# Optimization experiments

Hardware: AMD Instinct MI355X
Metric: run time of the kernel (lower is better)

Reference implementation:

```python
import jax, jax.numpy as jnp
import numpy as np

HID = 256
EDGE_F = 64
N_CELL = 4096
N_EDGE = 65536
BSZ = 4
EPS = 1e-5


def setup_inputs() -> dict:
    key = jax.random.key(0)
    ks = jax.random.split(key, 12)
    def lin(k, fan_in, fan_out):
        # torch Linear default init: U(-1/sqrt(fan_in), 1/sqrt(fan_in))
        bound = 1.0 / np.sqrt(fan_in)
        kw, kb = jax.random.split(k)
        W = jax.random.uniform(kw, (fan_in, fan_out), jnp.float32, -bound, bound)
        b = jax.random.uniform(kb, (fan_out,), jnp.float32, -bound, bound)
        return W, b
    cell_x = jax.random.normal(ks[0], (BSZ, N_CELL, HID), jnp.float32)
    edge_index = jax.random.randint(ks[1], (BSZ, N_EDGE, 2), 0, N_CELL, jnp.int64)
    edge_attr = jax.random.normal(ks[2], (BSZ, N_EDGE, EDGE_F), jnp.float32)
    mW1, mb1 = lin(ks[3], HID + EDGE_F, HID)
    mW2, mb2 = lin(ks[4], HID, HID)
    uW1, ub1 = lin(ks[5], 2 * HID, HID)
    uW2, ub2 = lin(ks[6], HID, HID)
    gamma = jnp.ones((HID,), jnp.float32)
    beta = jnp.zeros((HID,), jnp.float32)
    return {"cell_x": cell_x, "edge_index": edge_index, "edge_attr": edge_attr,
            "mW1": mW1, "mb1": mb1, "mW2": mW2, "mb2": mb2,
            "uW1": uW1, "ub1": ub1, "uW2": uW2, "ub2": ub2,
            "gamma": gamma, "beta": beta}


def reference(cell_x, edge_index, edge_attr, mW1, mb1, mW2, mb2,
              uW1, ub1, uW2, ub2, gamma, beta):
    n_cell = cell_x.shape[1]
    src = jnp.clip(edge_index[..., 0], 0, n_cell - 1)  # [B, E]
    dst = jnp.clip(edge_index[..., 1], 0, n_cell - 1)  # [B, E]

    # gather source node features per edge: [B, E, H]
    src_x = jnp.take_along_axis(cell_x, src[..., None], axis=1)

    # edge message MLP
    m_in = jnp.concatenate([src_x, edge_attr], axis=-1)  # [B, E, H+F]
    msg = jax.nn.relu(m_in @ mW1 + mb1) @ mW2 + mb2      # [B, E, H]

    # mean aggregation at destination nodes (scatter-add + count)
    def agg_one(m, d):
        s = jax.ops.segment_sum(m, d, num_segments=n_cell)                    # [N, H]
        c = jax.ops.segment_sum(jnp.ones((d.shape[0],), m.dtype), d,
                                num_segments=n_cell)                          # [N]
        return s / jnp.maximum(c, 1.0)[:, None]
    agg = jax.vmap(agg_one)(msg, dst)  # [B, N, H]

    # node update MLP + residual LayerNorm
    u_in = jnp.concatenate([cell_x, agg], axis=-1)        # [B, N, 2H]
    out = jax.nn.relu(u_in @ uW1 + ub1) @ uW2 + ub2       # [B, N, H]
    h = cell_x + out
    mu = jnp.mean(h, axis=-1, keepdims=True)
    var = jnp.mean(jnp.square(h - mu), axis=-1, keepdims=True)
    return (h - mu) * jax.lax.rsqrt(var + EPS) * gamma + beta
```

## Files before the change

kernel.cpp:

```cpp
#include <hip/hip_runtime.h>

#define HID 256
#define EF  64
#define KIN 320
#define NC  4096
#define NE  65536
#define BSZ 4
#define EPSV 1e-5f

typedef unsigned short ushort_t;
typedef __attribute__((ext_vector_type(8))) short s16x8;
typedef __attribute__((ext_vector_type(16))) float f32x16;

#define EPAD 68
#define HPAD 260
#define UPAD 520
#define HSF  260

__device__ __forceinline__ ushort_t bf16_rne(float f) {
    unsigned u = __float_as_uint(f);
    return (ushort_t)((u + 0x7fffu + ((u >> 16) & 1u)) >> 16);
}
__device__ __forceinline__ float bf16_to_f(ushort_t u) {
    return __uint_as_float(((unsigned)u) << 16);
}
__device__ __forceinline__ void split_bf16(float v, ushort_t& h, ushort_t& l) {
    unsigned u = __float_as_uint(v);
    h = (ushort_t)(u >> 16);
    float hf = __uint_as_float(u & 0xffff0000u);
    l = (ushort_t)(__float_as_uint(v - hf) >> 16);
}

__device__ __forceinline__ void pack_one(const float* W, int idx,
                                         ushort_t* hi, ushort_t* lo) {
    int l = idx & 63;
    int tn = idx >> 6;
    int nt = tn & 7, t = tn >> 3;
    int k0 = t * 16 + (l >> 5) * 8;
    int col = nt * 32 + (l & 31);
    #pragma unroll
    for (int j = 0; j < 8; ++j) {
        float v = W[(size_t)(k0 + j) * 256 + col];
        ushort_t h, lw;
        split_bf16(v, h, lw);
        hi[(size_t)idx * 8 + j] = h;
        lo[(size_t)idx * 8 + j] = lw;
    }
}

#define FR1 10240
#define FR2 8192
#define PACK1B 104
#define FUSEB 256
#define ZEROB 256

__global__ __launch_bounds__(256)
void prep_kernel(const float* __restrict__ mW1, const float* __restrict__ uW1,
                 const float* __restrict__ uW2, const float* __restrict__ mW2,
                 const float* __restrict__ ub1, const float* __restrict__ mb2,
                 ushort_t* __restrict__ w1hi, ushort_t* __restrict__ w1lo,
                 ushort_t* __restrict__ u1hi, ushort_t* __restrict__ u1lo,
                 ushort_t* __restrict__ u2hi, ushort_t* __restrict__ u2lo,
                 float* __restrict__ W2u, float* __restrict__ bias2u,
                 float4* __restrict__ zp, int n4) {
    int bid = blockIdx.x;
    if (bid < PACK1B) {
        int idx = bid * 256 + threadIdx.x;
        if (idx < FR1) { pack_one(mW1, idx, w1hi, w1lo); return; }
        idx -= FR1;
        if (idx < FR2) { pack_one(uW1, idx, u1hi, u1lo); return; }
        idx -= FR2;
        pack_one(uW2, idx, u2hi, u2lo);
        return;
    }
    bid -= PACK1B;
    if (bid < FUSEB) {
        int k = bid, n = threadIdx.x;
        const float* wrow = mW2 + (size_t)k * 256;
        float acc = 0.f;
        #pragma unroll 8
        for (int m = 0; m < 256; ++m)
            acc = fmaf(wrow[m], uW1[(size_t)(256 + m) * 256 + n], acc);
        W2u[(size_t)k * 256 + n] = acc;
        return;
    }
    bid -= FUSEB;
    if (bid == 0) {
        int n = threadIdx.x;
        float acc = ub1[n];
        #pragma unroll 8
        for (int m = 0; m < 256; ++m)
            acc = fmaf(mb2[m], uW1[(size_t)(256 + m) * 256 + n], acc);
        bias2u[n] = acc;
        return;
    }
    bid -= 1;
    int i = bid * 256 + threadIdx.x;
    int stride = ZEROB * 256;
    float4 z = make_float4(0.f, 0.f, 0.f, 0.f);
    for (; i < n4; i += stride) zp[i] = z;
}

__global__ __launch_bounds__(256)
void hist_kernel(const int* __restrict__ eidx, float* __restrict__ counts) {
    int i = blockIdx.x * 256 + threadIdx.x;
    int b = i >> 16;
    int2 v = ((const int2*)eidx)[i];
    int d = min(max(v.y, 0), NC - 1);
    atomicAdd(&counts[b * NC + d], 1.0f);
}

__global__ __launch_bounds__(1024)
void scan_kernel(const float* __restrict__ counts, int* __restrict__ woff,
                 const float* __restrict__ W2u,
                 ushort_t* __restrict__ w2uhi, ushort_t* __restrict__ w2ulo) {
    if (blockIdx.x >= BSZ) {
        if (threadIdx.x < 256) {
            int idx = (blockIdx.x - BSZ) * 256 + threadIdx.x;
            pack_one(W2u, idx, w2uhi, w2ulo);
        }
        return;
    }
    __shared__ int wsum[16];
    int b = blockIdx.x, t = threadIdx.x;
    int base = b * NC + t * 4;
    int v0 = (int)counts[base],     v1 = (int)counts[base + 1];
    int v2 = (int)counts[base + 2], v3 = (int)counts[base + 3];
    int ts = v0 + v1 + v2 + v3;
    int lane = t & 63;
    int x = ts;
    #pragma unroll
    for (int off = 1; off < 64; off <<= 1) {
        int y = __shfl_up(x, off, 64);
        if (lane >= off) x += y;
    }
    if (lane == 63) wsum[t >> 6] = x;
    __syncthreads();
    if (t == 0) {
        int s = 0;
        #pragma unroll
        for (int w = 0; w < 16; ++w) { int tmp = wsum[w]; wsum[w] = s; s += tmp; }
    }
    __syncthreads();
    int excl = wsum[t >> 6] + (x - ts);
    woff[base]     = excl;
    woff[base + 1] = excl + v0;
    woff[base + 2] = excl + v0 + v1;
    woff[base + 3] = excl + v0 + v1 + v2;
}

__global__ __launch_bounds__(256)
void scatter_kernel(const int* __restrict__ eidx, int* __restrict__ woff,
                    int* __restrict__ sorted) {
    int i = blockIdx.x * 256 + threadIdx.x;
    int b = i >> 16, e = i & (NE - 1);
    int2 v = ((const int2*)eidx)[i];
    int d = min(max(v.y, 0), NC - 1);
    int pos = atomicAdd(&woff[b * NC + d], 1);
    sorted[(size_t)b * NE + pos] = e;
}

__global__ __launch_bounds__(512, 6)
void pre_kernel(const float* __restrict__ cell_x,
                const ushort_t* __restrict__ w1hi, const ushort_t* __restrict__ w1lo,
                const ushort_t* __restrict__ u1hi, const ushort_t* __restrict__ u1lo,
                float* __restrict__ Pe, ushort_t* __restrict__ Pn) {
    __shared__ ushort_t Us[32 * HPAD];

    const int tid = threadIdx.x;
    const size_t r0 = (size_t)blockIdx.x * 32;
    const int wv = tid >> 6, ln = tid & 63;
    const int m32 = ln & 31, half = ln >> 5;
    const int col = wv * 32 + m32;

    const ushort_t* wph = w1hi + ((size_t)wv * 64 + ln) * 8;
    const ushort_t* wpl = w1lo + ((size_t)wv * 64 + ln) * 8;
    const ushort_t* uph = u1hi + ((size_t)wv * 64 + ln) * 8;
    const ushort_t* upl = u1lo + ((size_t)wv * 64 + ln) * 8;
    s16x8 wh = *(const s16x8*)wph, wl = *(const s16x8*)wpl;
    s16x8 uh = *(const s16x8*)uph, ul = *(const s16x8*)upl;

    {
        const int row = tid >> 4, c8 = tid & 15;
        const float4* crow = (const float4*)(cell_x + (r0 + row) * HID);
        #pragma unroll
        for (int i = 0; i < 4; ++i) {
            int c = c8 + i * 16;
            float4 v = crow[c];
            *(ushort4*)&Us[row * HPAD + c * 4] =
                make_ushort4(bf16_rne(v.x), bf16_rne(v.y), bf16_rne(v.z), bf16_rne(v.w));
        }
    }
    __syncthreads();

    f32x16 aw, au;
    #pragma unroll
    for (int r = 0; r < 16; ++r) { aw[r] = 0.f; au[r] = 0.f; }

    #pragma unroll 2
    for (int t = 0; t < 16; ++t) {
        int tn = (t + 1 < 16) ? t + 1 : 15;
        s16x8 whn = *(const s16x8*)(wph + (size_t)tn * 4096);
        s16x8 wln = *(const s16x8*)(wpl + (size_t)tn * 4096);
        s16x8 uhn = *(const s16x8*)(uph + (size_t)tn * 4096);
        s16x8 uln = *(const s16x8*)(upl + (size_t)tn * 4096);
        s16x8 a = *(const s16x8*)&Us[m32 * HPAD + t * 16 + half * 8];
        aw = __builtin_amdgcn_mfma_f32_32x32x16_bf16(a, wh, aw, 0, 0, 0);
        aw = __builtin_amdgcn_mfma_f32_32x32x16_bf16(a, wl, aw, 0, 0, 0);
        au = __builtin_amdgcn_mfma_f32_32x32x16_bf16(a, uh, au, 0, 0, 0);
        au = __builtin_amdgcn_mfma_f32_32x32x16_bf16(a, ul, au, 0, 0, 0);
        wh = whn; wl = wln; uh = uhn; ul = uln;
    }

    #pragma unroll
    for (int r = 0; r < 16; ++r) {
        int row = (r & 3) + 8 * (r >> 2) + 4 * half;
        Pe[(r0 + row) * 256 + col] = aw[r];
        Pn[(r0 + row) * 256 + col] = bf16_rne(au[r]);
    }
}

__global__ __launch_bounds__(512, 4)
void edge_kernel(const float* __restrict__ Pe,
                 const int*   __restrict__ eidx,
                 const int*   __restrict__ sorted,
                 const float* __restrict__ eattr,
                 const ushort_t* __restrict__ w1hi, const ushort_t* __restrict__ w1lo,
                 const float* __restrict__ b1,
                 float* __restrict__ aggf) {
    __shared__ ushort_t Xs[64 * EPAD];
    __shared__ int s_src[64], s_dst[64], s_eid[64];

    const int tid = threadIdx.x;
    const int b   = blockIdx.x >> 10;
    const int e0  = (blockIdx.x & 1023) * 64;
    const int wv = tid >> 6, ln = tid & 63;
    const int m32 = ln & 31, half = ln >> 5;
    const int col = wv * 32 + m32;

    if (tid < 64) {
        int eid = sorted[(size_t)b * NE + e0 + tid];
        s_eid[tid] = eid;
        int2 v = ((const int2*)eidx)[(size_t)b * NE + eid];
        s_src[tid] = min(max(v.x, 0), NC - 1);
        s_dst[tid] = min(max(v.y, 0), NC - 1);
    }

    const ushort_t* ph = w1hi + ((size_t)(16 * 8 + wv) * 64 + ln) * 8;
    const ushort_t* pl = w1lo + ((size_t)(16 * 8 + wv) * 64 + ln) * 8;
    s16x8 bh0 = *(const s16x8*)ph;
    s16x8 bl0 = *(const s16x8*)pl;
    s16x8 bh1 = *(const s16x8*)(ph + 4096);
    s16x8 bl1 = *(const s16x8*)(pl + 4096);
    s16x8 bh2 = *(const s16x8*)(ph + 8192);
    s16x8 bl2 = *(const s16x8*)(pl + 8192);
    s16x8 bh3 = *(const s16x8*)(ph + 12288);
    s16x8 bl3 = *(const s16x8*)(pl + 12288);

    __syncthreads();

    float t0[16], t1[16];
    {
        const float* pb = Pe + (size_t)b * NC * 256 + col;
        #pragma unroll
        for (int r = 0; r < 16; ++r) {
            int rw = (r & 3) + 8 * (r >> 2) + 4 * half;
            t0[r] = pb[(size_t)s_src[rw] * 256];
            t1[r] = pb[(size_t)s_src[rw + 32] * 256];
        }
    }

    {
        const int row = tid >> 3, c8 = tid & 7;
        const float4* arow = (const float4*)(eattr + ((size_t)b * NE + s_eid[row]) * EF);
        #pragma unroll
        for (int i = 0; i < 2; ++i) {
            int c = c8 + i * 8;
            float4 v = arow[c];
            *(ushort4*)&Xs[row * EPAD + c * 4] =
                make_ushort4(bf16_rne(v.x), bf16_rne(v.y), bf16_rne(v.z), bf16_rne(v.w));
        }
    }
    __syncthreads();

    f32x16 A0, A1;
    {
        float bias = b1[col];
        #pragma unroll
        for (int r = 0; r < 16; ++r) { A0[r] = bias; A1[r] = bias; }
    }
    {
        int ao = m32 * EPAD + half * 8;
        s16x8 a0, a1;
        a0 = *(const s16x8*)&Xs[ao];      a1 = *(const s16x8*)&Xs[ao + 32 * EPAD];
        A0 = __builtin_amdgcn_mfma_f32_32x32x16_bf16(a0, bh0, A0, 0, 0, 0);
        A0 = __builtin_amdgcn_mfma_f32_32x32x16_bf16(a0, bl0, A0, 0, 0, 0);
        A1 = __builtin_amdgcn_mfma_f32_32x32x16_bf16(a1, bh0, A1, 0, 0, 0);
        A1 = __builtin_amdgcn_mfma_f32_32x32x16_bf16(a1, bl0, A1, 0, 0, 0);
        a0 = *(const s16x8*)&Xs[ao + 16]; a1 = *(const s16x8*)&Xs[ao + 16 + 32 * EPAD];
        A0 = __builtin_amdgcn_mfma_f32_32x32x16_bf16(a0, bh1, A0, 0, 0, 0);
        A0 = __builtin_amdgcn_mfma_f32_32x32x16_bf16(a0, bl1, A0, 0, 0, 0);
        A1 = __builtin_amdgcn_mfma_f32_32x32x16_bf16(a1, bh1, A1, 0, 0, 0);
        A1 = __builtin_amdgcn_mfma_f32_32x32x16_bf16(a1, bl1, A1, 0, 0, 0);
        a0 = *(const s16x8*)&Xs[ao + 32]; a1 = *(const s16x8*)&Xs[ao + 32 + 32 * EPAD];
        A0 = __builtin_amdgcn_mfma_f32_32x32x16_bf16(a0, bh2, A0, 0, 0, 0);
        A0 = __builtin_amdgcn_mfma_f32_32x32x16_bf16(a0, bl2, A0, 0, 0, 0);
        A1 = __builtin_amdgcn_mfma_f32_32x32x16_bf16(a1, bh2, A1, 0, 0, 0);
        A1 = __builtin_amdgcn_mfma_f32_32x32x16_bf16(a1, bl2, A1, 0, 0, 0);
        a0 = *(const s16x8*)&Xs[ao + 48]; a1 = *(const s16x8*)&Xs[ao + 48 + 32 * EPAD];
        A0 = __builtin_amdgcn_mfma_f32_32x32x16_bf16(a0, bh3, A0, 0, 0, 0);
        A0 = __builtin_amdgcn_mfma_f32_32x32x16_bf16(a0, bl3, A0, 0, 0, 0);
        A1 = __builtin_amdgcn_mfma_f32_32x32x16_bf16(a1, bh3, A1, 0, 0, 0);
        A1 = __builtin_amdgcn_mfma_f32_32x32x16_bf16(a1, bl3, A1, 0, 0, 0);
    }

    #pragma unroll
    for (int r = 0; r < 16; ++r) {
        A0[r] = fmaxf(A0[r] + t0[r], 0.f);
        A1[r] = fmaxf(A1[r] + t1[r], 0.f);
    }

    {
        const int l31 = ln & 31;
        int dl = s_dst[l31];
        int dp = (l31 == 0) ? ~dl : s_dst[l31 - 1];
        unsigned m = (unsigned)__ballot(dl != dp);
        unsigned rem = m & ~1u;
        int lo = 0;
        while (lo < 32) {
            int hi = rem ? (int)__builtin_ctz(rem) : 32;
            rem &= rem - 1;
            int d = __shfl(dl, lo, 64);
            float s = 0.f;
            #pragma unroll
            for (int r = 0; r < 16; ++r) {
                int row = (r & 3) + 8 * (r >> 2) + 4 * half;
                s += (row >= lo && row < hi) ? A0[r] : 0.f;
            }
            s += __shfl_xor(s, 32, 64);
            if (ln < 32) atomicAdd(&aggf[((size_t)b * NC + d) * HID + col], s);
            lo = hi;
        }
        dl = s_dst[32 + l31];
        dp = (l31 == 0) ? ~dl : s_dst[32 + l31 - 1];
        m = (unsigned)__ballot(dl != dp);
        rem = m & ~1u;
        lo = 0;
        while (lo < 32) {
            int hi = rem ? (int)__builtin_ctz(rem) : 32;
            rem &= rem - 1;
            int d = __shfl(dl, lo, 64);
            float s = 0.f;
            #pragma unroll
            for (int r = 0; r < 16; ++r) {
                int row = (r & 3) + 8 * (r >> 2) + 4 * half;
                s += (row >= lo && row < hi) ? A1[r] : 0.f;
            }
            s += __shfl_xor(s, 32, 64);
            if (ln < 32) atomicAdd(&aggf[((size_t)b * NC + d) * HID + col], s);
            lo = hi;
        }
    }
}

__global__ __launch_bounds__(512, 6)
void node_kernel(const float* __restrict__ cell_x,
                 const float* __restrict__ aggf,
                 const float* __restrict__ counts,
                 const ushort_t* __restrict__ Pn,
                 const ushort_t* __restrict__ w2uhi, const ushort_t* __restrict__ w2ulo,
                 const float* __restrict__ bias2u,
                 const ushort_t* __restrict__ u2hi, const ushort_t* __restrict__ u2lo,
                 const float* __restrict__ b2,
                 const float* __restrict__ gamma, const float* __restrict__ beta,
                 float* __restrict__ out) {
    __shared__ ushort_t Us[32 * UPAD];
    __shared__ float s_inv[32];
    float* hs = (float*)Us;

    const int tid = threadIdx.x;
    const int b   = blockIdx.x >> 7;
    const int r0  = (blockIdx.x & 127) * 32;
    const int wv = tid >> 6, ln = tid & 63;
    const int m32 = ln & 31, half = ln >> 5;
    const int col = wv * 32 + m32;

    const ushort_t* b1ph = w2uhi + ((size_t)wv * 64 + ln) * 8;
    const ushort_t* b1pl = w2ulo + ((size_t)wv * 64 + ln) * 8;
    s16x8 bhi = *(const s16x8*)b1ph;
    s16x8 blo = *(const s16x8*)b1pl;

    if (tid < 32) {
        float c = counts[b * NC + r0 + tid];
        s_inv[tid] = 1.0f / fmaxf(c, 1.0f);
    }

    ushort_t pnt[16];
    {
        const ushort_t* pb = Pn + ((size_t)b * NC + r0) * 256 + col;
        #pragma unroll
        for (int r = 0; r < 16; ++r) {
            int row = (r & 3) + 8 * (r >> 2) + 4 * half;
            pnt[r] = pb[(size_t)row * 256];
        }
    }
    __syncthreads();

    {
        const int row = tid >> 4, c8 = tid & 15;
        const float4* grow = (const float4*)(aggf + ((size_t)b * NC + r0 + row) * HID);
        float inv = s_inv[row];
        #pragma unroll
        for (int i = 0; i < 4; ++i) {
            int c = c8 + i * 16;
            float4 g = grow[c];
            *(ushort4*)&Us[row * HPAD + c * 4] =
                make_ushort4(bf16_rne(g.x * inv), bf16_rne(g.y * inv),
                             bf16_rne(g.z * inv), bf16_rne(g.w * inv));
        }
    }
    __syncthreads();

    f32x16 acc;
    {
        float bias = bias2u[col];
        #pragma unroll
        for (int r = 0; r < 16; ++r) acc[r] = bias;
    }
    #pragma unroll 2
    for (int t = 0; t < 16; ++t) {
        int tn1 = (t + 1 < 16) ? t + 1 : 15;
        s16x8 bhin = *(const s16x8*)(b1ph + (size_t)tn1 * 4096);
        s16x8 blon = *(const s16x8*)(b1pl + (size_t)tn1 * 4096);
        s16x8 a = *(const s16x8*)&Us[m32 * HPAD + t * 16 + half * 8];
        acc = __builtin_amdgcn_mfma_f32_32x32x16_bf16(a, bhi, acc, 0, 0, 0);
        acc = __builtin_amdgcn_mfma_f32_32x32x16_bf16(a, blo, acc, 0, 0, 0);
        bhi = bhin; blo = blon;
    }

    #pragma unroll
    for (int r = 0; r < 16; ++r) acc[r] += bf16_to_f(pnt[r]);

    const ushort_t* b2ph = u2hi + ((size_t)wv * 64 + ln) * 8;
    const ushort_t* b2pl = u2lo + ((size_t)wv * 64 + ln) * 8;
    bhi = *(const s16x8*)b2ph;
    blo = *(const s16x8*)b2pl;

    __syncthreads();

    #pragma unroll
    for (int r = 0; r < 16; ++r) {
        int row = (r & 3) + 8 * (r >> 2) + 4 * half;
        Us[row * HPAD + col] = bf16_rne(fmaxf(acc[r], 0.f));
    }
    __syncthreads();

    float cxt[16];
    #pragma unroll
    for (int r = 0; r < 16; ++r) {
        int row = (r & 3) + 8 * (r >> 2) + 4 * half;
        cxt[r] = cell_x[((size_t)b * NC + r0 + row) * HID + col];
    }

    f32x16 c2;
    {
        float bias = b2[col];
        #pragma unroll
        for (int r = 0; r < 16; ++r) c2[r] = bias;
    }
    #pragma unroll 2
    for (int t = 0; t < 16; ++t) {
        int tn1 = (t + 1 < 16) ? t + 1 : 15;
        s16x8 bhin = *(const s16x8*)(b2ph + (size_t)tn1 * 4096);
        s16x8 blon = *(const s16x8*)(b2pl + (size_t)tn1 * 4096);
        s16x8 a = *(const s16x8*)&Us[m32 * HPAD + t * 16 + half * 8];
        c2 = __builtin_amdgcn_mfma_f32_32x32x16_bf16(a, bhi, c2, 0, 0, 0);
        c2 = __builtin_amdgcn_mfma_f32_32x32x16_bf16(a, blo, c2, 0, 0, 0);
        bhi = bhin; blo = blon;
    }
    __syncthreads();

    #pragma unroll
    for (int r = 0; r < 16; ++r) {
        int row = (r & 3) + 8 * (r >> 2) + 4 * half;
        hs[row * HSF + col] = c2[r] + cxt[r];
    }
    __syncthreads();

    #pragma unroll
    for (int i = 0; i < 4; ++i) {
        int r = wv * 4 + i;
        float v[4];
        float s = 0.f, q = 0.f;
        #pragma unroll
        for (int j = 0; j < 4; ++j) {
            v[j] = hs[r * HSF + ln + 64 * j];
            s += v[j];
            q = fmaf(v[j], v[j], q);
        }
        #pragma unroll
        for (int off = 32; off > 0; off >>= 1) {
            s += __shfl_xor(s, off, 64);
            q += __shfl_xor(q, off, 64);
        }
        float mu = s * (1.0f / HID);
        float var = q * (1.0f / HID) - mu * mu;
        float rs = rsqrtf(var + EPSV);
        float* orow = out + ((size_t)b * NC + r0 + r) * HID;
        #pragma unroll
        for (int j = 0; j < 4; ++j) {
            int c = ln + 64 * j;
            orow[c] = (v[j] - mu) * rs * gamma[c] + beta[c];
        }
    }
}

extern "C" void kernel_launch(void* const* d_in, const int* in_sizes, int n_in,
                              void* d_out, int out_size, void* d_ws, size_t ws_size,
                              hipStream_t stream) {
    const float* cell_x = (const float*)d_in[0];
    const int*   eidx   = (const int*)d_in[1];
    const float* eattr  = (const float*)d_in[2];
    const float* mW1    = (const float*)d_in[3];
    const float* mb1    = (const float*)d_in[4];
    const float* mW2    = (const float*)d_in[5];
    const float* mb2    = (const float*)d_in[6];
    const float* uW1    = (const float*)d_in[7];
    const float* ub1    = (const float*)d_in[8];
    const float* uW2    = (const float*)d_in[9];
    const float* ub2    = (const float*)d_in[10];
    const float* gamma  = (const float*)d_in[11];
    const float* beta   = (const float*)d_in[12];
    float* out = (float*)d_out;

    float* aggf   = (float*)d_ws;
    float* counts = aggf + (size_t)BSZ * NC * HID;
    int*   woff   = (int*)(counts + BSZ * NC);
    int*   sorted = woff + BSZ * NC;
    ushort_t* w1hi = (ushort_t*)(sorted + (size_t)BSZ * NE);
    ushort_t* w1lo = w1hi + KIN * HID;
    ushort_t* u1hi = w1lo + KIN * HID;
    ushort_t* u1lo = u1hi + HID * HID;
    ushort_t* u2hi = u1lo + HID * HID;
    ushort_t* u2lo = u2hi + HID * HID;
    ushort_t* w2uhi = u2lo + HID * HID;
    ushort_t* w2ulo = w2uhi + HID * HID;
    float*    W2u   = (float*)(w2ulo + HID * HID);
    float*    bias2u = W2u + HID * HID;
    float*    Pe   = bias2u + HID;
    ushort_t* Pn   = (ushort_t*)(Pe + (size_t)BSZ * NC * 256);

    int n4 = (BSZ * NC * HID * 4 + BSZ * NC * 4) / 16;
    prep_kernel<<<PACK1B + FUSEB + 1 + ZEROB, 256, 0, stream>>>(
        mW1, uW1, uW2, mW2, ub1, mb2,
        w1hi, w1lo, u1hi, u1lo, u2hi, u2lo, W2u, bias2u, (float4*)d_ws, n4);
    hist_kernel<<<BSZ * NE / 256, 256, 0, stream>>>(eidx, counts);
    scan_kernel<<<BSZ + 32, 1024, 0, stream>>>(counts, woff, W2u, w2uhi, w2ulo);
    scatter_kernel<<<BSZ * NE / 256, 256, 0, stream>>>(eidx, woff, sorted);
    pre_kernel<<<BSZ * NC / 32, 512, 0, stream>>>(cell_x, w1hi, w1lo, u1hi, u1lo, Pe, Pn);
    edge_kernel<<<BSZ * NE / 64, 512, 0, stream>>>(Pe, eidx, sorted, eattr,
                                                   w1hi, w1lo, mb1, aggf);
    node_kernel<<<BSZ * NC / 32, 512, 0, stream>>>(cell_x, aggf, counts, Pn,
                                                   w2uhi, w2ulo, bias2u,
                                                   u2hi, u2lo, ub2,
                                                   gamma, beta, out);
}
```

Before: 271.8 us.

## Fuse edge message and node update kernels with shared-memory aggregation per node tile

Combines the edge kernel and node kernel into one kernel where each block owns 32 destination nodes and loops over their dst-sorted edges in chunks of 64. Messages are reduced into a shared-memory accumulator instead of global atomics, so the global aggregation buffer and its zeroing and read-back go away. In exchange, each block's work now depends on the in-degree of its 32 nodes (load imbalance, a serial chunk loop), and parallelism drops from 4096 edge blocks to 512 node blocks.

Result: slower. 300.9 us (+10.7%).

```diff
diff --git a/kernel.cpp b/kernel.cpp
--- a/kernel.cpp
+++ b/kernel.cpp
@@ -14,8 +14,7 @@
 
 #define EPAD 68
 #define HPAD 260
-#define UPAD 520
-#define HSF  260
+#define AGGP 258
 
 __device__ __forceinline__ ushort_t bf16_rne(float f) {
     unsigned u = __float_as_uint(f);
@@ -52,7 +51,7 @@
 #define FR2 8192
 #define PACK1B 104
 #define FUSEB 256
-#define ZEROB 256
+#define ZEROB 16
 
 __global__ __launch_bounds__(256)
 void prep_kernel(const float* __restrict__ mW1, const float* __restrict__ uW1,
@@ -221,29 +220,38 @@
 }
 
 __global__ __launch_bounds__(512, 4)
-void edge_kernel(const float* __restrict__ Pe,
-                 const int*   __restrict__ eidx,
-                 const int*   __restrict__ sorted,
-                 const float* __restrict__ eattr,
-                 const ushort_t* __restrict__ w1hi, const ushort_t* __restrict__ w1lo,
-                 const float* __restrict__ b1,
-                 float* __restrict__ aggf) {
-    __shared__ ushort_t Xs[64 * EPAD];
-    __shared__ int s_src[64], s_dst[64], s_eid[64];
+void fused_kernel(const float* __restrict__ cell_x,
+                  const int*   __restrict__ eidx,
+                  const int*   __restrict__ sorted,
+                  const int*   __restrict__ woff,
+                  const float* __restrict__ eattr,
+                  const float* __restrict__ counts,
+                  const float* __restrict__ Pe,
+                  const ushort_t* __restrict__ Pn,
+                  const ushort_t* __restrict__ w1hi, const ushort_t* __restrict__ w1lo,
+                  const float* __restrict__ b1,
+                  const ushort_t* __restrict__ w2uhi, const ushort_t* __restrict__ w2ulo,
+                  const float* __restrict__ bias2u,
+                  const ushort_t* __restrict__ u2hi, const ushort_t* __restrict__ u2lo,
+                  const float* __restrict__ b2,
+                  const float* __restrict__ gamma, const float* __restrict__ beta,
+                  float* __restrict__ out) {
+    __shared__ float aggL[32 * AGGP];
+    __shared__ ushort_t pool[32 * HPAD];
+    __shared__ int s_eid[64], s_src[64], s_dstL[64];
+    __shared__ float s_inv[32];
 
     const int tid = threadIdx.x;
-    const int b   = blockIdx.x >> 10;
-    const int e0  = (blockIdx.x & 1023) * 64;
+    const int b   = blockIdx.x >> 7;
+    const int r0  = (blockIdx.x & 127) * 32;
     const int wv = tid >> 6, ln = tid & 63;
     const int m32 = ln & 31, half = ln >> 5;
     const int col = wv * 32 + m32;
 
-    if (tid < 64) {
-        int eid = sorted[(size_t)b * NE + e0 + tid];
-        s_eid[tid] = eid;
-        int2 v = ((const int2*)eidx)[(size_t)b * NE + eid];
-        s_src[tid] = min(max(v.x, 0), NC - 1);
-        s_dst[tid] = min(max(v.y, 0), NC - 1);
+    for (int i = tid; i < 32 * AGGP; i += 512) aggL[i] = 0.f;
+    if (tid < 32) {
+        float c = counts[b * NC + r0 + tid];
+        s_inv[tid] = 1.0f / fmaxf(c, 1.0f);
     }
 
     const ushort_t* ph = w1hi + ((size_t)(16 * 8 + wv) * 64 + ln) * 8;
@@ -257,168 +265,157 @@
     s16x8 bh3 = *(const s16x8*)(ph + 12288);
     s16x8 bl3 = *(const s16x8*)(pl + 12288);
 
-    __syncthreads();
-
-    float t0[16], t1[16];
-    {
-        const float* pb = Pe + (size_t)b * NC * 256 + col;
-        #pragma unroll
-        for (int r = 0; r < 16; ++r) {
-            int rw = (r & 3) + 8 * (r >> 2) + 4 * half;
-            t0[r] = pb[(size_t)s_src[rw] * 256];
-            t1[r] = pb[(size_t)s_src[rw + 32] * 256];
-        }
-    }
-
-    {
-        const int row = tid >> 3, c8 = tid & 7;
-        const float4* arow = (const float4*)(eattr + ((size_t)b * NE + s_eid[row]) * EF);
-        #pragma unroll
-        for (int i = 0; i < 2; ++i) {
-            int c = c8 + i * 8;
-            float4 v = arow[c];
-            *(ushort4*)&Xs[row * EPAD + c * 4] =
-                make_ushort4(bf16_rne(v.x), bf16_rne(v.y), bf16_rne(v.z), bf16_rne(v.w));
-        }
-    }
-    __syncthreads();
-
-    f32x16 A0, A1;
-    {
-        float bias = b1[col];
-        #pragma unroll
-        for (int r = 0; r < 16; ++r) { A0[r] = bias; A1[r] = bias; }
-    }
-    {
-        int ao = m32 * EPAD + half * 8;
-        s16x8 a0, a1;
-        a0 = *(const s16x8*)&Xs[ao];      a1 = *(const s16x8*)&Xs[ao + 32 * EPAD];
-        A0 = __builtin_amdgcn_mfma_f32_32x32x16_bf16(a0, bh0, A0, 0, 0, 0);
-        A0 = __builtin_amdgcn_mfma_f32_32x32x16_bf16(a0, bl0, A0, 0, 0, 0);
-        A1 = __builtin_amdgcn_mfma_f32_32x32x16_bf16(a1, bh0, A1, 0, 0, 0);
-        A1 = __builtin_amdgcn_mfma_f32_32x32x16_bf16(a1, bl0, A1, 0, 0, 0);
-        a0 = *(const s16x8*)&Xs[ao + 16]; a1 = *(const s16x8*)&Xs[ao + 16 + 32 * EPAD];
-        A0 = __builtin_amdgcn_mfma_f32_32x32x16_bf16(a0, bh1, A0, 0, 0, 0);
-        A0 = __builtin_amdgcn_mfma_f32_32x32x16_bf16(a0, bl1, A0, 0, 0, 0);
-        A1 = __builtin_amdgcn_mfma_f32_32x32x16_bf16(a1, bh1, A1, 0, 0, 0);
-        A1 = __builtin_amdgcn_mfma_f32_32x32x16_bf16(a1, bl1, A1, 0, 0, 0);
-        a0 = *(const s16x8*)&Xs[ao + 32]; a1 = *(const s16x8*)&Xs[ao + 32 + 32 * EPAD];
-        A0 = __builtin_amdgcn_mfma_f32_32x32x16_bf16(a0, bh2, A0, 0, 0, 0);
-        A0 = __builtin_amdgcn_mfma_f32_32x32x16_bf16(a0, bl2, A0, 0, 0, 0);
-        A1 = __builtin_amdgcn_mfma_f32_32x32x16_bf16(a1, bh2, A1, 0, 0, 0);
-        A1 = __builtin_amdgcn_mfma_f32_32x32x16_bf16(a1, bl2, A1, 0, 0, 0);
-        a0 = *(const s16x8*)&Xs[ao + 48]; a1 = *(const s16x8*)&Xs[ao + 48 + 32 * EPAD];
-        A0 = __builtin_amdgcn_mfma_f32_32x32x16_bf16(a0, bh3, A0, 0, 0, 0);
-        A0 = __builtin_amdgcn_mfma_f32_32x32x16_bf16(a0, bl3, A0, 0, 0, 0);
-        A1 = __builtin_amdgcn_mfma_f32_32x32x16_bf16(a1, bh3, A1, 0, 0, 0);
-        A1 = __builtin_amdgcn_mfma_f32_32x32x16_bf16(a1, bl3, A1, 0, 0, 0);
-    }
-
-    #pragma unroll
-    for (int r = 0; r < 16; ++r) {
-        A0[r] = fmaxf(A0[r] + t0[r], 0.f);
-        A1[r] = fmaxf(A1[r] + t1[r], 0.f);
-    }
-
-    {
-        const int l31 = ln & 31;
-        int dl = s_dst[l31];
-        int dp = (l31 == 0) ? ~dl : s_dst[l31 - 1];
-        unsigned m = (unsigned)__ballot(dl != dp);
-        unsigned rem = m & ~1u;
-        int lo = 0;
-        while (lo < 32) {
-            int hi = rem ? (int)__builtin_ctz(rem) : 32;
-            rem &= rem - 1;
-            int d = __shfl(dl, lo, 64);
-            float s = 0.f;
+    const float biasE = b1[col];
+
+    const int basebin = b * NC + r0;
+    const int estart = (r0 == 0) ? 0 : woff[basebin - 1];
+    const int eend   = woff[basebin + 31];
+
+    __syncthreads();
+
+    for (int ch = estart; ch < eend; ch += 64) {
+        if (tid < 64) {
+            int idx = ch + tid;
+            bool valid = idx < eend;
+            int eid = sorted[(size_t)b * NE + (valid ? idx : eend - 1)];
+            s_eid[tid] = eid;
+            int2 v = ((const int2*)eidx)[(size_t)b * NE + eid];
+            s_src[tid] = min(max(v.x, 0), NC - 1);
+            s_dstL[tid] = valid ? (min(max(v.y, 0), NC - 1) - r0) : 1000;
+        }
+        __syncthreads();
+
+        float t0[16], t1[16];
+        {
+            const float* pb = Pe + (size_t)b * NC * 256 + col;
             #pragma unroll
             for (int r = 0; r < 16; ++r) {
-                int row = (r & 3) + 8 * (r >> 2) + 4 * half;
-                s += (row >= lo && row < hi) ? A0[r] : 0.f;
+                int rw = (r & 3) + 8 * (r >> 2) + 4 * half;
+                t0[r] = pb[(size_t)s_src[rw] * 256];
+                t1[r] = pb[(size_t)s_src[rw + 32] * 256];
             }
-            s += __shfl_xor(s, 32, 64);
-            if (ln < 32) atomicAdd(&aggf[((size_t)b * NC + d) * HID + col], s);
-            lo = hi;
-        }
-        dl = s_dst[32 + l31];
-        dp = (l31 == 0) ? ~dl : s_dst[32 + l31 - 1];
-        m = (unsigned)__ballot(dl != dp);
-        rem = m & ~1u;
-        lo = 0;
-        while (lo < 32) {
-            int hi = rem ? (int)__builtin_ctz(rem) : 32;
-            rem &= rem - 1;
-            int d = __shfl(dl, lo, 64);
-            float s = 0.f;
+        }
+
+        {
+            const int row = tid >> 3, c8 = tid & 7;
+            const float4* arow = (const float4*)(eattr + ((size_t)b * NE + s_eid[row]) * EF);
             #pragma unroll
-            for (int r = 0; r < 16; ++r) {
-                int row = (r & 3) + 8 * (r >> 2) + 4 * half;
-                s += (row >= lo && row < hi) ? A1[r] : 0.f;
+            for (int i = 0; i < 2; ++i) {
+                int c = c8 + i * 8;
+                float4 v = arow[c];
+                *(ushort4*)&pool[row * EPAD + c * 4] =
+                    make_ushort4(bf16_rne(v.x), bf16_rne(v.y), bf16_rne(v.z), bf16_rne(v.w));
             }
-            s += __shfl_xor(s, 32, 64);
-            if (ln < 32) atomicAdd(&aggf[((size_t)b * NC + d) * HID + col], s);
-            lo = hi;
-        }
-    }
-}
-
-__global__ __launch_bounds__(512, 6)
-void node_kernel(const float* __restrict__ cell_x,
-                 const float* __restrict__ aggf,
-                 const float* __restrict__ counts,
-                 const ushort_t* __restrict__ Pn,
-                 const ushort_t* __restrict__ w2uhi, const ushort_t* __restrict__ w2ulo,
-                 const float* __restrict__ bias2u,
-                 const ushort_t* __restrict__ u2hi, const ushort_t* __restrict__ u2lo,
-                 const float* __restrict__ b2,
-                 const float* __restrict__ gamma, const float* __restrict__ beta,
-                 float* __restrict__ out) {
-    __shared__ ushort_t Us[32 * UPAD];
-    __shared__ float s_inv[32];
-    float* hs = (float*)Us;
-
-    const int tid = threadIdx.x;
-    const int b   = blockIdx.x >> 7;
-    const int r0  = (blockIdx.x & 127) * 32;
-    const int wv = tid >> 6, ln = tid & 63;
-    const int m32 = ln & 31, half = ln >> 5;
-    const int col = wv * 32 + m32;
+        }
+        __syncthreads();
+
+        f32x16 A0, A1;
+        #pragma unroll
+        for (int r = 0; r < 16; ++r) { A0[r] = biasE; A1[r] = biasE; }
+        {
+            int ao = m32 * EPAD + half * 8;
+            s16x8 a0, a1;
+            a0 = *(const s16x8*)&pool[ao];      a1 = *(const s16x8*)&pool[ao + 32 * EPAD];
+            A0 = __builtin_amdgcn_mfma_f32_32x32x16_bf16(a0, bh0, A0, 0, 0, 0);
+            A0 = __builtin_amdgcn_mfma_f32_32x32x16_bf16(a0, bl0, A0, 0, 0, 0);
+            A1 = __builtin_amdgcn_mfma_f32_32x32x16_bf16(a1, bh0, A1, 0, 0, 0);
+            A1 = __builtin_amdgcn_mfma_f32_32x32x16_bf16(a1, bl0, A1, 0, 0, 0);
+            a0 = *(const s16x8*)&pool[ao + 16]; a1 = *(const s16x8*)&pool[ao + 16 + 32 * EPAD];
+            A0 = __builtin_amdgcn_mfma_f32_32x32x16_bf16(a0, bh1, A0, 0, 0, 0);
+            A0 = __builtin_amdgcn_mfma_f32_32x32x16_bf16(a0, bl1, A0, 0, 0, 0);
+            A1 = __builtin_amdgcn_mfma_f32_32x32x16_bf16(a1, bh1, A1, 0, 0, 0);
+            A1 = __builtin_amdgcn_mfma_f32_32x32x16_bf16(a1, bl1, A1, 0, 0, 0);
+            a0 = *(const s16x8*)&pool[ao + 32]; a1 = *(const s16x8*)&pool[ao + 32 + 32 * EPAD];
+            A0 = __builtin_amdgcn_mfma_f32_32x32x16_bf16(a0, bh2, A0, 0, 0, 0);
+            A0 = __builtin_amdgcn_mfma_f32_32x32x16_bf16(a0, bl2, A0, 0, 0, 0);
+            A1 = __builtin_amdgcn_mfma_f32_32x32x16_bf16(a1, bh2, A1, 0, 0, 0);
+            A1 = __builtin_amdgcn_mfma_f32_32x32x16_bf16(a1, bl2, A1, 0, 0, 0);
+            a0 = *(const s16x8*)&pool[ao + 48]; a1 = *(const s16x8*)&pool[ao + 48 + 32 * EPAD];
+            A0 = __builtin_amdgcn_mfma_f32_32x32x16_bf16(a0, bh3, A0, 0, 0, 0);
+            A0 = __builtin_amdgcn_mfma_f32_32x32x16_bf16(a0, bl3, A0, 0, 0, 0);
+            A1 = __builtin_amdgcn_mfma_f32_32x32x16_bf16(a1, bh3, A1, 0, 0, 0);
+            A1 = __builtin_amdgcn_mfma_f32_32x32x16_bf16(a1, bl3, A1, 0, 0, 0);
+        }
+
+        #pragma unroll
+        for (int r = 0; r < 16; ++r) {
+            A0[r] = fmaxf(A0[r] + t0[r], 0.f);
+            A1[r] = fmaxf(A1[r] + t1[r], 0.f);
+        }
+
+        {
+            const int l31 = ln & 31;
+            int dl = s_dstL[l31];
+            int dp = (l31 == 0) ? ~dl : s_dstL[l31 - 1];
+            unsigned m = (unsigned)__ballot(dl != dp);
+            unsigned rem = m & ~1u;
+            int lo = 0;
+            while (lo < 32) {
+                int hi = rem ? (int)__builtin_ctz(rem) : 32;
+                rem &= rem - 1;
+                int d = __shfl(dl, lo, 64);
+                float s = 0.f;
+                #pragma unroll
+                for (int r = 0; r < 16; ++r) {
+                    int row = (r & 3) + 8 * (r >> 2) + 4 * half;
+                    s += (row >= lo && row < hi) ? A0[r] : 0.f;
+                }
+                s += __shfl_xor(s, 32, 64);
+                if (ln < 32 && d < 32) atomicAdd(&aggL[d * AGGP + col], s);
+                lo = hi;
+            }
+            dl = s_dstL[32 + l31];
+            dp = (l31 == 0) ? ~dl : s_dstL[32 + l31 - 1];
+            m = (unsigned)__ballot(dl != dp);
+            rem = m & ~1u;
+            lo = 0;
+            while (lo < 32) {
+                int hi = rem ? (int)__builtin_ctz(rem) : 32;
+                rem &= rem - 1;
+                int d = __shfl(dl, lo, 64);
+                float s = 0.f;
+                #pragma unroll
+                for (int r = 0; r < 16; ++r) {
+                    int row = (r & 3) + 8 * (r >> 2) + 4 * half;
+                    s += (row >= lo && row < hi) ? A1[r] : 0.f;
+                }
+                s += __shfl_xor(s, 32, 64);
+                if (ln < 32 && d < 32) atomicAdd(&aggL[d * AGGP + col], s);
+                lo = hi;
+            }
+        }
+        __syncthreads();
+    }
+
+    ushort_t pnt[16];
+    {
+        const ushort_t* pb = Pn + ((size_t)b * NC + r0) * 256 + col;
+        #pragma unroll
+        for (int r = 0; r < 16; ++r) {
+            int row = (r & 3) + 8 * (r >> 2) + 4 * half;
+            pnt[r] = pb[(size_t)row * 256];
+        }
+    }
+
+    {
+        const int row = tid & 31, cg = tid >> 5;
+        float inv = s_inv[row];
+        #pragma unroll
+        for (int i = 0; i < 4; ++i) {
+            int c = cg + i * 16;
+            float2 g0 = *(const float2*)&aggL[row * AGGP + c * 4];
+            float2 g1 = *(const float2*)&aggL[row * AGGP + c * 4 + 2];
+            *(ushort4*)&pool[row * HPAD + c * 4] =
+                make_ushort4(bf16_rne(g0.x * inv), bf16_rne(g0.y * inv),
+                             bf16_rne(g1.x * inv), bf16_rne(g1.y * inv));
+        }
+    }
 
     const ushort_t* b1ph = w2uhi + ((size_t)wv * 64 + ln) * 8;
     const ushort_t* b1pl = w2ulo + ((size_t)wv * 64 + ln) * 8;
     s16x8 bhi = *(const s16x8*)b1ph;
     s16x8 blo = *(const s16x8*)b1pl;
 
-    if (tid < 32) {
-        float c = counts[b * NC + r0 + tid];
-        s_inv[tid] = 1.0f / fmaxf(c, 1.0f);
-    }
-
-    ushort_t pnt[16];
-    {
-        const ushort_t* pb = Pn + ((size_t)b * NC + r0) * 256 + col;
-        #pragma unroll
-        for (int r = 0; r < 16; ++r) {
-            int row = (r & 3) + 8 * (r >> 2) + 4 * half;
-            pnt[r] = pb[(size_t)row * 256];
-        }
-    }
-    __syncthreads();
-
-    {
-        const int row = tid >> 4, c8 = tid & 15;
-        const float4* grow = (const float4*)(aggf + ((size_t)b * NC + r0 + row) * HID);
-        float inv = s_inv[row];
-        #pragma unroll
-        for (int i = 0; i < 4; ++i) {
-            int c = c8 + i * 16;
-            float4 g = grow[c];
-            *(ushort4*)&Us[row * HPAD + c * 4] =
-                make_ushort4(bf16_rne(g.x * inv), bf16_rne(g.y * inv),
-                             bf16_rne(g.z * inv), bf16_rne(g.w * inv));
-        }
-    }
     __syncthreads();
 
     f32x16 acc;
@@ -432,7 +429,7 @@
         int tn1 = (t + 1 < 16) ? t + 1 : 15;
         s16x8 bhin = *(const s16x8*)(b1ph + (size_t)tn1 * 4096);
         s16x8 blon = *(const s16x8*)(b1pl + (size_t)tn1 * 4096);
-        s16x8 a = *(const s16x8*)&Us[m32 * HPAD + t * 16 + half * 8];
+        s16x8 a = *(const s16x8*)&pool[m32 * HPAD + t * 16 + half * 8];
         acc = __builtin_amdgcn_mfma_f32_32x32x16_bf16(a, bhi, acc, 0, 0, 0);
         acc = __builtin_amdgcn_mfma_f32_32x32x16_bf16(a, blo, acc, 0, 0, 0);
         bhi = bhin; blo = blon;
@@ -451,7 +448,7 @@
     #pragma unroll
     for (int r = 0; r < 16; ++r) {
         int row = (r & 3) + 8 * (r >> 2) + 4 * half;
-        Us[row * HPAD + col] = bf16_rne(fmaxf(acc[r], 0.f));
+        pool[row * HPAD + col] = bf16_rne(fmaxf(acc[r], 0.f));
     }
     __syncthreads();
 
@@ -473,17 +470,17 @@
         int tn1 = (t + 1 < 16) ? t + 1 : 15;
         s16x8 bhin = *(const s16x8*)(b2ph + (size_t)tn1 * 4096);
         s16x8 blon = *(const s16x8*)(b2pl + (size_t)tn1 * 4096);
-        s16x8 a = *(const s16x8*)&Us[m32 * HPAD + t * 16 + half * 8];
+        s16x8 a = *(const s16x8*)&pool[m32 * HPAD + t * 16 + half * 8];
         c2 = __builtin_amdgcn_mfma_f32_32x32x16_bf16(a, bhi, c2, 0, 0, 0);
         c2 = __builtin_amdgcn_mfma_f32_32x32x16_bf16(a, blo, c2, 0, 0, 0);
         bhi = bhin; blo = blon;
     }
-    __syncthreads();
-
+
+    float* hs = aggL;
     #pragma unroll
     for (int r = 0; r < 16; ++r) {
         int row = (r & 3) + 8 * (r >> 2) + 4 * half;
-        hs[row * HSF + col] = c2[r] + cxt[r];
+        hs[row * AGGP + col] = c2[r] + cxt[r];
     }
     __syncthreads();
 
@@ -494,7 +491,7 @@
         float s = 0.f, q = 0.f;
         #pragma unroll
         for (int j = 0; j < 4; ++j) {
-            v[j] = hs[r * HSF + ln + 64 * j];
+            v[j] = hs[r * AGGP + ln + 64 * j];
             s += v[j];
             q = fmaf(v[j], v[j], q);
         }
@@ -533,8 +530,7 @@
     const float* beta   = (const float*)d_in[12];
     float* out = (float*)d_out;
 
-    float* aggf   = (float*)d_ws;
-    float* counts = aggf + (size_t)BSZ * NC * HID;
+    float* counts = (float*)d_ws;
     int*   woff   = (int*)(counts + BSZ * NC);
     int*   sorted = woff + BSZ * NC;
     ushort_t* w1hi = (ushort_t*)(sorted + (size_t)BSZ * NE);
@@ -550,18 +546,18 @@
     float*    Pe   = bias2u + HID;
     ushort_t* Pn   = (ushort_t*)(Pe + (size_t)BSZ * NC * 256);
 
-    int n4 = (BSZ * NC * HID * 4 + BSZ * NC * 4) / 16;
+    int n4 = (BSZ * NC * 4) / 16;
     prep_kernel<<<PACK1B + FUSEB + 1 + ZEROB, 256, 0, stream>>>(
         mW1, uW1, uW2, mW2, ub1, mb2,
-        w1hi, w1lo, u1hi, u1lo, u2hi, u2lo, W2u, bias2u, (float4*)d_ws, n4);
+        w1hi, w1lo, u1hi, u1lo, u2hi, u2lo, W2u, bias2u, (float4*)counts, n4);
     hist_kernel<<<BSZ * NE / 256, 256, 0, stream>>>(eidx, counts);
     scan_kernel<<<BSZ + 32, 1024, 0, stream>>>(counts, woff, W2u, w2uhi, w2ulo);
     scatter_kernel<<<BSZ * NE / 256, 256, 0, stream>>>(eidx, woff, sorted);
     pre_kernel<<<BSZ * NC / 32, 512, 0, stream>>>(cell_x, w1hi, w1lo, u1hi, u1lo, Pe, Pn);
-    edge_kernel<<<BSZ * NE / 64, 512, 0, stream>>>(Pe, eidx, sorted, eattr,
-                                                   w1hi, w1lo, mb1, aggf);
-    node_kernel<<<BSZ * NC / 32, 512, 0, stream>>>(cell_x, aggf, counts, Pn,
-                                                   w2uhi, w2ulo, bias2u,
-                                                   u2hi, u2lo, ub2,
-                                                   gamma, beta, out);
-}
+    fused_kernel<<<BSZ * NC / 32, 512, 0, stream>>>(cell_x, eidx, sorted, woff, eattr,
+                                                    counts, Pe, Pn,
+                                                    w1hi, w1lo, mb1,
+                                                    w2uhi, w2ulo, bias2u,
+                                                    u2hi, u2lo, ub2,
+                                                    gamma, beta, out);
+}
```
